# Kernel optimization log

Hardware: AMD Instinct MI355X
Metric: run time of the kernel (lower is better)

## Reference

```python
import jax, jax.numpy as jnp
import numpy as np
from itertools import combinations

ADD = 3  # max subset size (init arg `add`)


def setup_inputs() -> dict:
    key = jax.random.key(0)
    k1, _ = jax.random.split(key)
    # fuzzy membership values in [0, 1]
    x = jax.random.uniform(k1, (131072, 16), dtype=jnp.float32)
    lambda_ = jnp.asarray(0.3, dtype=jnp.float32)  # learnable scalar parameter
    return {"x": x, "lambda_": lambda_}


def reference(x, lambda_):
    """Dubois t-norm over all column subsets of size 2..ADD.

    Vectorized per subset size k: gather all C(n, k) subsets at once
    ([B, Ck, k]) and fold the binary Dubois t-norm
        T(a, b) = a*b / max(max(a, b), lambda)
    over the k axis, instead of looping per combination.
    """
    n = x.shape[1]
    outs = [x]  # order matches original: identity columns first, then k=2, k=3, ...
    for k in range(2, ADD + 1):
        idx = np.array(list(combinations(range(n), k)), dtype=np.int32)  # [Ck, k]
        subset = x[:, idx]  # [B, Ck, k]
        hidden = subset[:, :, 0]
        for i in range(1, k):  # fold over subset elements (left-to-right, as original)
            s = subset[:, :, i]
            hidden = hidden * s / jnp.maximum(jnp.maximum(hidden, s), lambda_)
        outs.append(hidden)
    return jnp.concatenate(outs, axis=1)  # [B, n + sum_k C(n,k)] = [B, 696]
```

## Files before the change

### kernel.cpp

```cpp
#include <hip/hip_runtime.h>

#define NCOLS 16
#define NPAIR 120
#define NTRIP 560
#define OUTC  (NCOLS + NPAIR + NTRIP)
#define WPB   4

struct Tables {
    unsigned short pair_ij[NPAIR];
    unsigned short trip[NTRIP];
};

constexpr Tables make_tables() {
    Tables t{};
    int p = 0;
    for (int i = 0; i < NCOLS; ++i)
        for (int j = i + 1; j < NCOLS; ++j)
            t.pair_ij[p++] = (unsigned short)(i | (j << 8));
    int q = 0;
    for (int i = 0; i < NCOLS; ++i)
        for (int j = i + 1; j < NCOLS; ++j)
            for (int k = j + 1; k < NCOLS; ++k) {
                int pid = i * (2 * NCOLS - i - 1) / 2 + (j - i - 1);
                t.trip[q++] = (unsigned short)(pid | (k << 8));
            }
    return t;
}

__device__ const Tables d_tbl = make_tables();

__device__ __forceinline__ float tnorm(float a, float b, float lam) {
    float m = fmaxf(fmaxf(a, b), lam);
    return a * b * __builtin_amdgcn_rcpf(m);
}

__global__ __launch_bounds__(256) void dubois_kernel(
    const float* __restrict__ x, const float* __restrict__ lam_p,
    float* __restrict__ out, int B, int iters, int nwaves)
{
    __shared__ float s_x[WPB][NCOLS];
    __shared__ float s_pair[WPB][NPAIR];

    const int lane = threadIdx.x & 63;
    const int ws   = threadIdx.x >> 6;
    const int gwave = blockIdx.x * WPB + ws;
    const float lam = lam_p[0];

    for (int it = 0; it < iters; ++it) {
        const int row = gwave + it * nwaves;
        const bool active = row < B;

        if (active && lane < NCOLS) {
            float v = x[(size_t)row * NCOLS + lane];
            s_x[ws][lane] = v;
            out[(size_t)row * OUTC + lane] = v;
        }
        __syncthreads();

        if (active) {
            float* orow = out + (size_t)row * OUTC;
            #pragma unroll
            for (int r = 0; r < 2; ++r) {
                int p = lane + r * 64;
                if (p < NPAIR) {
                    unsigned int ij = d_tbl.pair_ij[p];
                    float a = s_x[ws][ij & 15];
                    float b = s_x[ws][ij >> 8];
                    float v = tnorm(a, b, lam);
                    s_pair[ws][p] = v;
                    orow[NCOLS + p] = v;
                }
            }
        }
        __syncthreads();

        if (active) {
            float* orow = out + (size_t)row * OUTC;
            #pragma unroll
            for (int r = 0; r < 9; ++r) {
                int t = lane + r * 64;
                if (t < NTRIP) {
                    unsigned int pk = d_tbl.trip[t];
                    float a = s_pair[ws][pk & 255];
                    float c = s_x[ws][pk >> 8];
                    orow[NCOLS + NPAIR + t] = tnorm(a, c, lam);
                }
            }
        }
        __syncthreads();
    }
}

extern "C" void kernel_launch(void* const* d_in, const int* in_sizes, int n_in,
                              void* d_out, int out_size, void* d_ws, size_t ws_size,
                              hipStream_t stream) {
    const float* x   = (const float*)d_in[0];
    const float* lam = (const float*)d_in[1];
    float* out = (float*)d_out;

    const int B = in_sizes[0] / NCOLS;
    const int blocks = 2048;
    const int nwaves = blocks * WPB;
    const int iters  = (B + nwaves - 1) / nwaves;

    dubois_kernel<<<blocks, 256, 0, stream>>>(x, lam, out, B, iters, nwaves);
}
```

Baseline: 404.9 us.

## Replace shared-memory staging with wave shuffles and per-lane column tables

Removes shared memory and the three block-wide barriers per row. Each lane now keeps a register-cached table entry for each of its 11 output columns, gathers inputs with wave shuffles, and computes each triple directly from the three raw values rather than reusing stored pair results. All outputs, identity columns included, are written in one unified loop. This adds redundant t-norm work per column and more shuffles, in exchange for removing synchronisation and shared-memory traffic in a store-bound kernel.

```diff
diff --git a/kernel.cpp b/kernel.cpp
--- a/kernel.cpp
+++ b/kernel.cpp
@@ -4,30 +4,27 @@
 #define NPAIR 120
 #define NTRIP 560
 #define OUTC  (NCOLS + NPAIR + NTRIP)
-#define WPB   4
+#define NREG  11
 
-struct Tables {
-    unsigned short pair_ij[NPAIR];
-    unsigned short trip[NTRIP];
-};
+struct ColTab { unsigned int c[NREG * 64]; };
 
-constexpr Tables make_tables() {
-    Tables t{};
-    int p = 0;
+constexpr ColTab make_cols() {
+    ColTab t{};
+    int q = 0;
+    for (int i = 0; i < NCOLS; ++i)
+        t.c[q++] = (unsigned)i | ((unsigned)i << 8) | ((unsigned)i << 16) | (0u << 24);
     for (int i = 0; i < NCOLS; ++i)
         for (int j = i + 1; j < NCOLS; ++j)
-            t.pair_ij[p++] = (unsigned short)(i | (j << 8));
-    int q = 0;
+            t.c[q++] = (unsigned)i | ((unsigned)j << 8) | ((unsigned)j << 16) | (1u << 24);
     for (int i = 0; i < NCOLS; ++i)
         for (int j = i + 1; j < NCOLS; ++j)
-            for (int k = j + 1; k < NCOLS; ++k) {
-                int pid = i * (2 * NCOLS - i - 1) / 2 + (j - i - 1);
-                t.trip[q++] = (unsigned short)(pid | (k << 8));
-            }
+            for (int k = j + 1; k < NCOLS; ++k)
+                t.c[q++] = (unsigned)i | ((unsigned)j << 8) | ((unsigned)k << 16) | (2u << 24);
+    while (q < NREG * 64) t.c[q++] = 0u;
     return t;
 }
 
-__device__ const Tables d_tbl = make_tables();
+__device__ const ColTab d_cols = make_cols();
 
 __device__ __forceinline__ float tnorm(float a, float b, float lam) {
     float m = fmaxf(fmaxf(a, b), lam);
@@ -38,56 +35,41 @@
     const float* __restrict__ x, const float* __restrict__ lam_p,
     float* __restrict__ out, int B, int iters, int nwaves)
 {
-    __shared__ float s_x[WPB][NCOLS];
-    __shared__ float s_pair[WPB][NPAIR];
+    const int lane  = threadIdx.x & 63;
+    const int gwave = (blockIdx.x * blockDim.x + threadIdx.x) >> 6;
+    const float lam = lam_p[0];
 
-    const int lane = threadIdx.x & 63;
-    const int ws   = threadIdx.x >> 6;
-    const int gwave = blockIdx.x * WPB + ws;
-    const float lam = lam_p[0];
+    unsigned int tab[NREG];
+    #pragma unroll
+    for (int r = 0; r < NREG; ++r)
+        tab[r] = d_cols.c[lane + r * 64];
 
     for (int it = 0; it < iters; ++it) {
         const int row = gwave + it * nwaves;
-        const bool active = row < B;
+        if (row >= B) break;
 
-        if (active && lane < NCOLS) {
-            float v = x[(size_t)row * NCOLS + lane];
-            s_x[ws][lane] = v;
-            out[(size_t)row * OUTC + lane] = v;
+        float v = x[(size_t)row * NCOLS + (lane & 15)];
+        float* __restrict__ orow = out + (size_t)row * OUTC;
+
+        float res[NREG];
+        #pragma unroll
+        for (int r = 0; r < NREG; ++r) {
+            unsigned int e = tab[r];
+            float a  = __shfl(v, (int)(e & 255u));
+            float b  = __shfl(v, (int)((e >> 8) & 255u));
+            float c  = __shfl(v, (int)((e >> 16) & 255u));
+            float t1 = tnorm(a, b, lam);
+            float t2 = tnorm(t1, c, lam);
+            unsigned int op = e >> 24;
+            res[r] = (op == 0u) ? a : ((op == 1u) ? t1 : t2);
         }
-        __syncthreads();
 
-        if (active) {
-            float* orow = out + (size_t)row * OUTC;
-            #pragma unroll
-            for (int r = 0; r < 2; ++r) {
-                int p = lane + r * 64;
-                if (p < NPAIR) {
-                    unsigned int ij = d_tbl.pair_ij[p];
-                    float a = s_x[ws][ij & 15];
-                    float b = s_x[ws][ij >> 8];
-                    float v = tnorm(a, b, lam);
-                    s_pair[ws][p] = v;
-                    orow[NCOLS + p] = v;
-                }
-            }
+        #pragma unroll
+        for (int r = 0; r < NREG; ++r) {
+            int c = lane + r * 64;
+            if (r < NREG - 1 || c < OUTC)
+                orow[c] = res[r];
         }
-        __syncthreads();
-
-        if (active) {
-            float* orow = out + (size_t)row * OUTC;
-            #pragma unroll
-            for (int r = 0; r < 9; ++r) {
-                int t = lane + r * 64;
-                if (t < NTRIP) {
-                    unsigned int pk = d_tbl.trip[t];
-                    float a = s_pair[ws][pk & 255];
-                    float c = s_x[ws][pk >> 8];
-                    orow[NCOLS + NPAIR + t] = tnorm(a, c, lam);
-                }
-            }
-        }
-        __syncthreads();
     }
 }
 
@@ -99,9 +81,10 @@
     float* out = (float*)d_out;
 
     const int B = in_sizes[0] / NCOLS;
-    const int blocks = 2048;
-    const int nwaves = blocks * WPB;
-    const int iters  = (B + nwaves - 1) / nwaves;
+    const int threads = 256;
+    const int blocks  = 2048;
+    const int nwaves  = blocks * (threads / 64);
+    const int iters   = (B + nwaves - 1) / nwaves;
 
-    dubois_kernel<<<blocks, 256, 0, stream>>>(x, lam, out, B, iters, nwaves);
+    dubois_kernel<<<blocks, threads, 0, stream>>>(x, lam, out, B, iters, nwaves);
 }
```

Measured after the change: 397.8 us. No clear change (-1.8%).
